# Optimization experiments

Measured on AMD Instinct MI355X. Metric: run time of the kernel, lower is better.

Reference implementation:

```python
import jax, jax.numpy as jnp
import numpy as np

B, V, S = 128, 64, 40
D, H, VOC = 256, 256, 20000


def setup_inputs() -> dict:
    key = jax.random.key(0)
    ks = jax.random.split(key, 26)
    g = lambda k, shp: (jax.random.normal(k, shp, dtype=jnp.float32) * 0.02)
    inp = {}
    inp['input_seqs'] = jax.random.randint(ks[0], (B, V, S), 0, VOC + 1)
    inp['mask'] = jnp.zeros((B, V), jnp.float32)
    inp['length'] = jax.random.randint(ks[1], (B,), 1, V + 1)
    inp['seq_time_step'] = jax.random.uniform(ks[2], (B, V), dtype=jnp.float32)
    inp['codemask'] = jnp.zeros((B, V, S), jnp.float32)
    inp['label'] = jax.random.randint(ks[3], (B,), 0, 2)
    # embedding table; padding_idx=-1 in torch == row VOC zeroed
    inp['emb'] = g(ks[4], (VOC + 1, D)).at[VOC].set(0.0)
    # LSTM (single layer, batch_first): torch gate order i,f,g,o
    inp['W_ih'] = g(ks[5], (4 * H, D))
    inp['W_hh'] = g(ks[6], (4 * H, H))
    inp['b_ih'] = g(ks[7], (4 * H,))
    inp['b_hh'] = g(ks[8], (4 * H,))
    # attention projections
    inp['Whk'] = g(ks[9], (D, H))
    inp['bhk'] = g(ks[10], (D,))
    inp['W1'] = g(ks[11], (64, 2 * H))
    inp['b1'] = g(ks[12], (64,))
    inp['W2'] = g(ks[13], (2, 64))
    inp['b2'] = g(ks[14], (2,))
    # classifyer MLP: d -> 4d -> 2d -> 2
    inp['C1W'] = g(ks[15], (4 * D, D))
    inp['C1b'] = g(ks[16], (4 * D,))
    inp['C2W'] = g(ks[17], (2 * D, 4 * D))
    inp['C2b'] = g(ks[18], (2 * D,))
    inp['CoW'] = g(ks[19], (2, 2 * D))
    inp['Cob'] = g(ks[20], (2,))
    return inp


def _lstm(x, W_ih, W_hh, b_ih, b_hh):
    # x: [B,T,D] -> hs: [B,T,H]; torch gate order i,f,g,o
    Bsz = x.shape[0]
    Hd = W_hh.shape[1]
    xg = jnp.einsum('btd,gd->btg', x, W_ih) + b_ih + b_hh  # [B,T,4H]

    def step(carry, xg_t):
        h, c = carry
        gates = xg_t + h @ W_hh.T
        i, f, gg, o = jnp.split(gates, 4, axis=-1)
        i = jax.nn.sigmoid(i); f = jax.nn.sigmoid(f)
        gg = jnp.tanh(gg); o = jax.nn.sigmoid(o)
        c = f * c + i * gg
        h = o * jnp.tanh(c)
        return (h, c), h

    z = jnp.zeros((Bsz, Hd), x.dtype)
    _, hs = jax.lax.scan(step, (z, z), jnp.swapaxes(xg, 0, 1))
    return jnp.swapaxes(hs, 0, 1)


def _classify(h, C1W, C1b, C2W, C2b, CoW, Cob):
    h = jax.nn.relu(h @ C1W.T + C1b)
    h = jax.nn.relu(h @ C2W.T + C2b)
    return h @ CoW.T + Cob


def reference(input_seqs, mask, length, seq_time_step, codemask, label,
              emb, W_ih, W_hh, b_ih, b_hh, Whk, bhk, W1, b1, W2, b2,
              C1W, C1b, C2W, C2b, CoW, Cob):
    # before(): embedding gather -> relu -> sum over codes (eval mode, no dropout)
    v = jax.nn.relu(emb[input_seqs]).sum(-2)  # [B,V,D]
    h = _lstm(v, W_ih, W_hh, b_ih, b_hh)       # [B,V,H]

    # vectorized form of the per-timestep attention loop:
    # bar_v[:,0]=v[:,0]; for i>=1: mix of e_k=v[:,0] and w_hk(h[:,i-1])
    e_k = v[:, :1, :]                                   # [B,1,D]
    wh = h @ Whk.T + bhk                                # [B,V,D]
    wh_prev = wh[:, :-1, :]                             # [B,V-1,D] (h at i-1)
    e_b = jnp.broadcast_to(e_k, wh_prev.shape)
    cat = jnp.concatenate([e_b, wh_prev], axis=-1)      # [B,V-1,2D]
    attn = jax.nn.softmax(jnp.tanh(cat @ W1.T + b1) @ W2.T + b2, axis=-1)
    bar_rest = e_b * attn[..., 0:1] + wh_prev * attn[..., 1:2]
    bar_v = jnp.concatenate([v[:, :1, :], bar_rest], axis=1)  # [B,V,D]

    # GAN stand-in (external injected module): identity
    Dec_V, Gen_V = bar_v, bar_v
    gen_h = _lstm(Gen_V, W_ih, W_hh, b_ih, b_hh)

    og = _classify(h, C1W, C1b, C2W, C2b, CoW, Cob)        # [B,V,2]
    fake = _classify(gen_h, C1W, C1b, C2W, C2b, CoW, Cob)  # [B,V,2]
    final_og = og[:, -1, :]
    final_fake = fake[:, -1, :]
    return (final_og, final_fake, Dec_V, Gen_V, seq_time_step, label)
```

## Files before the change

### kernel.cpp

```cpp
#include <hip/hip_runtime.h>

#define DEV __device__ __forceinline__

typedef float f32x4 __attribute__((ext_vector_type(4)));
typedef short s16x8 __attribute__((ext_vector_type(8)));
typedef short s16x4 __attribute__((ext_vector_type(4)));

DEV unsigned short f2bf(float f){
  unsigned int u = __float_as_uint(f);
  u += 0x7fffu + ((u>>16)&1u);
  return (unsigned short)(u>>16);
}
DEV float bf2f(unsigned short h){ return __uint_as_float(((unsigned int)h)<<16); }

#if __has_builtin(__builtin_amdgcn_rcpf)
DEV float frcp_(float x){ return __builtin_amdgcn_rcpf(x); }
#else
DEV float frcp_(float x){ return 1.f/x; }
#endif
#if __has_builtin(__builtin_amdgcn_exp2f)
DEV float fexp2_(float x){ return __builtin_amdgcn_exp2f(x); }
#else
DEV float fexp2_(float x){ return exp2f(x); }
#endif

DEV float tanh_(float x){
  x = fminf(x, 30.f);
  float e = fexp2_(2.8853900817779268f*x);
  return (e-1.f)*frcp_(e+1.f);
}

DEV unsigned char f2e4m3(float x){
  unsigned int u = __float_as_uint(x);
  unsigned int s = (u>>24)&0x80u;
  unsigned int mag = u & 0x7fffffffu;
  if (mag > 0x43E00000u) mag = 0x43E00000u;
  mag += 0x000FFFFFu + ((mag>>20)&1u);
  int e = (int)(mag>>23) - 120;
  unsigned int m = (mag>>20)&7u;
  unsigned int r = (e<=0) ? 0u : (((unsigned)e<<3)|m);
  return (unsigned char)(s|r);
}

DEV f32x4 mfma_bf16(s16x8 a, s16x8 b, f32x4 c){
  return __builtin_amdgcn_mfma_f32_16x16x32_bf16(a,b,c,0,0,0);
}
DEV f32x4 mfma_fp8(long a, long b, f32x4 c){
  return __builtin_amdgcn_mfma_f32_16x16x32_fp8_fp8(a,b,c,0,0,0);
}

DEV void lds_barrier(){
  asm volatile("s_waitcnt lgkmcnt(0)\n\ts_barrier" ::: "memory");
}

DEV unsigned aload_rlx(unsigned* p){
  return __hip_atomic_load(p, __ATOMIC_RELAXED, __HIP_MEMORY_SCOPE_AGENT);
}
DEV void astore_rel(unsigned* p, unsigned v){
  __hip_atomic_store(p, v, __ATOMIC_RELEASE, __HIP_MEMORY_SCOPE_AGENT);
}
DEV void aadd_rel(unsigned* p, unsigned v){
  __hip_atomic_fetch_add(p, v, __ATOMIC_RELEASE, __HIP_MEMORY_SCOPE_AGENT);
}
DEV void acq_fence(){ __builtin_amdgcn_fence(__ATOMIC_ACQUIRE, "agent"); }
DEV void spin_rlx(unsigned* p, unsigned tgt){
  while (aload_rlx(p) < tgt) __builtin_amdgcn_s_sleep(8);
  asm volatile("" ::: "memory");
}
template<int FENCE>
DEV void block_wait_ge(unsigned* p, unsigned tgt){
  if (threadIdx.x == 0){
    spin_rlx(p, tgt);
    if (FENCE) acq_fence();
  }
  __syncthreads();
}
DEV s16x4 aload64(const unsigned short* p){
  unsigned long long v = __hip_atomic_load((unsigned long long*)(void*)p,
      __ATOMIC_RELAXED, __HIP_MEMORY_SCOPE_AGENT);
  union { unsigned long long u; s16x4 s; } c; c.u = v; return c.s;
}

#define Bx 128
#define Vx 64
#define Sx 40
#define Dx 256
#define Hx 256
#define NVOC 20001

#define OFF_OG   0
#define OFF_FAKE 256
#define OFF_DECV 512
#define OFF_GENV 2097664
#define OFF_STS  4194816
#define OFF_LBL  4203008

#define PW_IH  0
#define PW_HH  262144
#define PW_HK  524288
#define PW_1   589824
#define PC_1   622592
#define PC_2   884736
#define PC_O   1409024
#define P_TOT  1410048

#define HPB 264
#define WHP 272

#define FCT(t) ((t)*32)
#define FBV(t) (2048 + (t)*32)
#define FXG(t) (4096 + (t)*32)
#define FUC    6144
#define FTOT   8192

__global__ void k_cvt_emb(const float* __restrict__ emb, unsigned short* __restrict__ emb16){
  size_t i = (size_t)blockIdx.x*256 + threadIdx.x;
  emb16[i] = f2bf(emb[i]);
}

__global__ void k_pre(const int* __restrict__ seqs, const unsigned short* __restrict__ emb16,
                      unsigned short* __restrict__ v16,
                      float* __restrict__ decv, float* __restrict__ genv,
                      unsigned short* __restrict__ barv16,
                      const float* __restrict__ W_ih, const float* __restrict__ Whh,
                      const float* __restrict__ Whk, const float* __restrict__ W1,
                      const float* __restrict__ C1W, const float* __restrict__ C2W,
                      const float* __restrict__ CoW,
                      unsigned short* __restrict__ pool, unsigned char* __restrict__ whh8,
                      const float* __restrict__ sts, const int* __restrict__ label,
                      float* __restrict__ out, unsigned* __restrict__ flags){
  int bx = blockIdx.x, tid = threadIdx.x;
  if (bx < 8192){
    int bt = bx, d = tid;
    const int* sp = seqs + (size_t)bt*Sx;
    float acc = 0.f;
    #pragma unroll 8
    for (int s=0;s<Sx;s++) acc += fmaxf(bf2f(emb16[(size_t)sp[s]*Dx + d]), 0.f);
    size_t o = (size_t)bt*Dx + d;
    v16[o] = f2bf(acc);
    if ((bt & 63) == 0){ decv[o] = acc; genv[o] = acc; barv16[o] = f2bf(acc); }
    return;
  }
  if (bx < 14724){
    int i = (bx-8192)*256 + tid;
    if (i < P_TOT){
      float v;
      if      (i < PW_HH) v = W_ih[i - PW_IH];
      else if (i < PW_HK) v = Whh [i - PW_HH];
      else if (i < PW_1 ) v = Whk [i - PW_HK];
      else if (i < PC_1 ) v = W1  [i - PW_1 ];
      else if (i < PC_2 ) v = C1W [i - PC_1 ];
      else if (i < PC_O ) v = C2W [i - PC_2 ];
      else                v = CoW [i - PC_O ];
      pool[i] = f2bf(v);
    } else if (i < P_TOT + 262144){
      whh8[i - P_TOT] = f2e4m3(16.f*Whh[i - P_TOT]);
    }
    return;
  }
  for (int i=tid;i<FTOT;i+=256) flags[i] = (i==FBV(0)) ? 1u : 0u;
  for (int i=tid;i<Bx*Vx;i+=256) out[OFF_STS + i] = sts[i];
  if (tid < Bx) out[OFF_LBL + tid] = (float)label[tid];
}

template<int MODE_A, int MODE_C, int RELU>
__global__ void k_gemm(const unsigned short* __restrict__ A, const unsigned short* __restrict__ Bw,
                       const float* __restrict__ bias1, const float* __restrict__ bias2,
                       unsigned short* __restrict__ C, int K, int Ntot, float scale){
  int tid = threadIdx.x, w = tid>>6, l = tid&63, lm = l&15, q = l>>4;
  int m0 = blockIdx.x*64;
  int n0 = blockIdx.y*256 + w*64;
  f32x4 acc[4][4];
  #pragma unroll
  for (int nt=0;nt<4;nt++){
    int n = n0 + nt*16 + lm;
    float bz = bias1 ? bias1[n] : 0.f;
    if (bias2) bz += bias2[n];
    #pragma unroll
    for (int mt=0;mt<4;mt++) acc[mt][nt] = (f32x4){bz,bz,bz,bz};
  }
  const s16x8* Arow[4];
  #pragma unroll
  for (int mt=0;mt<4;mt++){
    int m = m0 + mt*16 + lm;
    size_t off = (MODE_A==0) ? (size_t)m*K : ((size_t)(m&127)*Vx + (m>>7))*(size_t)K;
    Arow[mt] = (const s16x8*)(A + off);
  }
  int kkn = K/32;
  for (int kk=0; kk<kkn; kk++){
    s16x8 bfr[4];
    #pragma unroll
    for (int nt=0;nt<4;nt++){
      int n = n0 + nt*16 + lm;
      bfr[nt] = *(const s16x8*)(Bw + (size_t)n*K + kk*32 + q*8);
    }
    #pragma unroll
    for (int mt=0;mt<4;mt++){
      s16x8 afr = Arow[mt][kk*4 + q];
      #pragma unroll
      for (int nt=0;nt<4;nt++)
        acc[mt][nt] = mfma_bf16(afr, bfr[nt], acc[mt][nt]);
    }
  }
  #pragma unroll
  for (int mt=0;mt<4;mt++){
    int mbase = m0 + mt*16 + q*4;
    #pragma unroll
    for (int nt=0;nt<4;nt++){
      int n = n0 + nt*16 + lm;
      if (MODE_C==0){
        #pragma unroll
        for (int r=0;r<4;r++){
          float val = scale*acc[mt][nt][r];
          if (RELU) val = fmaxf(val, 0.f);
          C[(size_t)(mbase+r)*Ntot + n] = f2bf(val);
        }
      } else {
        int tt = mbase>>7, bb = mbase&127;
        int gg = bb>>4;
        s16x4 sv;
        #pragma unroll
        for (int r=0;r<4;r++) sv[r] = (short)f2bf(scale*acc[mt][nt][r]);
        *(s16x4*)(C + (((size_t)tt*8 + gg)*1024 + n)*16 + (bb&15)) = sv;
      }
    }
  }
}

template<int IS1>
DEV void scan_body(unsigned char* hl, const unsigned char* __restrict__ W8,
                   const unsigned short* __restrict__ xg, unsigned short* __restrict__ hist,
                   int g, unsigned* __restrict__ flags){
  int tid = threadIdx.x;
  int w = tid>>6, l = tid&63, lm = l&15, q = l>>4;
  int j = w*16 + lm;
  for (int i=tid;i<2*16*HPB;i+=1024) hl[i] = 0;
  long Bf[4][8];
  #pragma unroll
  for (int qq=0;qq<4;qq++){
    int n = qq*256 + j;
    #pragma unroll
    for (int kk=0;kk<8;kk++)
      Bf[qq][kk] = *(const long*)(W8 + (size_t)n*256 + kk*32 + q*8);
  }
  float cst[4] = {0.f,0.f,0.f,0.f};
  const unsigned short* xgb = xg + (size_t)g*16384 + q*4;
  s16x4 xc[4], xn[4];
  if (!IS1) block_wait_ge<0>(&flags[FXG(0)], 1);
  #pragma unroll
  for (int qq=0;qq<4;qq++){
    const unsigned short* p = xgb + (qq*256+j)*16;
    xc[qq] = IS1 ? *(const s16x4*)p : aload64(p);
  }
  __syncthreads();
  const float K1 = 1.4426950408889634f/256.f;
  const unsigned char* hrd = hl + lm*HPB + q*8;
  #pragma unroll 1
  for (int t=0;t<Vx;t++){
    if (t < Vx-1){
      if (!IS1) block_wait_ge<0>(&flags[FXG(t+1)], 1);
      #pragma unroll
      for (int qq=0;qq<4;qq++){
        const unsigned short* p = xgb + (size_t)(t+1)*131072 + (qq*256+j)*16;
        xn[qq] = IS1 ? *(const s16x4*)p : aload64(p);
      }
    }
    const unsigned char* hb = hrd + (t&1)*(16*HPB);
    f32x4 a0, a1, a2, a3;
    #pragma unroll
    for (int r=0;r<4;r++){
      a0[r] = bf2f((unsigned short)xc[0][r]);
      a1[r] = bf2f((unsigned short)xc[1][r]);
      a2[r] = bf2f((unsigned short)xc[2][r]);
      a3[r] = bf2f((unsigned short)xc[3][r]);
    }
    #pragma unroll
    for (int kk=0;kk<8;kk++){
      long af = *(const long*)(hb + kk*32);
      a0 = mfma_fp8(af, Bf[0][kk], a0);
      a1 = mfma_fp8(af, Bf[1][kk], a1);
      a2 = mfma_fp8(af, Bf[2][kk], a2);
      a3 = mfma_fp8(af, Bf[3][kk], a3);
    }
    unsigned char* hn = hl + ((t+1)&1)*(16*HPB) + j;
    float hv16[4];
    #pragma unroll
    for (int r=0;r<4;r++){
      float iv = frcp_(1.f + fexp2_(-K1*a0[r]));
      float fv = frcp_(1.f + fexp2_(-K1*a1[r]));
      float eg = fexp2_(2.f*K1*a2[r]);
      float gv = (eg-1.f)*frcp_(eg+1.f);
      float ov = frcp_(1.f + fexp2_(-K1*a3[r]));
      float cv = fv*cst[r] + iv*gv;
      cst[r] = cv;
      float ec = fexp2_(2.8853900817779268f*fminf(cv,30.f));
      float hv = ov*(ec-1.f)*frcp_(ec+1.f);
      hv16[r] = 16.f*hv;
      if (IS1)
        hist[((size_t)t*Bx + g*16 + q*4 + r)*Hx + j] = f2bf(hv);
      else if (t==Vx-1)
        hist[((size_t)(g*16 + q*4 + r))*Hx + j] = f2bf(hv);
    }
#if __has_builtin(__builtin_amdgcn_cvt_pk_fp8_f32)
    int p01 = __builtin_amdgcn_cvt_pk_fp8_f32(hv16[0], hv16[1], 0, false);
    int p23 = __builtin_amdgcn_cvt_pk_fp8_f32(hv16[2], hv16[3], 0, false);
    hn[(q*4+0)*HPB] = (unsigned char)p01;
    hn[(q*4+1)*HPB] = (unsigned char)(p01>>8);
    hn[(q*4+2)*HPB] = (unsigned char)p23;
    hn[(q*4+3)*HPB] = (unsigned char)(p23>>8);
#else
    #pragma unroll
    for (int r=0;r<4;r++) hn[(q*4+r)*HPB] = f2e4m3(hv16[r]);
#endif
    #pragma unroll
    for (int qq=0;qq<4;qq++) xc[qq] = xn[qq];
    if (IS1){
      __syncthreads();
      if (tid == 0) aadd_rel(&flags[FCT(t)], 1);
    } else {
      lds_barrier();
    }
  }
}

DEV void worker_body(unsigned short* whs, int t,
    const unsigned short* __restrict__ hist1, const unsigned short* __restrict__ v16,
    const float* __restrict__ u, const unsigned short* __restrict__ pool,
    const float* __restrict__ bhk, const float* __restrict__ W2, const float* __restrict__ b2,
    const float* __restrict__ b_ih, const float* __restrict__ b_hh,
    float* __restrict__ decv, float* __restrict__ genv,
    unsigned short* __restrict__ barv16, unsigned short* __restrict__ xg2,
    unsigned* flags){
  int tid = threadIdx.x, w = tid>>6, l = tid&63, lm = l&15, q = l>>4;
  if (t < 63){
    block_wait_ge<1>(&flags[FCT(t)], 8);
    int r0 = (w&7)*16, n0 = (w>>3)*128;
    const s16x8* Arow = (const s16x8*)(hist1 + ((size_t)t*Bx + r0 + lm)*Hx);
    f32x4 acc[8];
    #pragma unroll
    for (int nt=0;nt<8;nt++){
      float bz = bhk[n0 + nt*16 + lm];
      acc[nt] = (f32x4){bz,bz,bz,bz};
    }
    #pragma unroll
    for (int kk=0;kk<8;kk++){
      s16x8 afr = Arow[kk*4 + q];
      #pragma unroll
      for (int nt=0;nt<8;nt++){
        int n = n0 + nt*16 + lm;
        s16x8 bfr = *(const s16x8*)(pool + PW_HK + (size_t)n*256 + kk*32 + q*8);
        acc[nt] = mfma_bf16(afr, bfr, acc[nt]);
      }
    }
    #pragma unroll
    for (int nt=0;nt<8;nt++){
      int n = n0 + nt*16 + lm, mb = r0 + q*4;
      #pragma unroll
      for (int r=0;r<4;r++) whs[(size_t)(mb+r)*WHP + n] = f2bf(acc[nt][r]);
    }
    if (tid == 0){ spin_rlx(&flags[FUC], 8); acq_fence(); }
    __syncthreads();
    if (w < 8){
      int m0l = w*16;
      f32x4 a2[4];
      #pragma unroll
      for (int nt=0;nt<4;nt++){
        int n = nt*16 + lm;
        #pragma unroll
        for (int r=0;r<4;r++) a2[nt][r] = u[(size_t)(m0l + q*4 + r)*64 + n];
      }
      #pragma unroll
      for (int kk=0;kk<8;kk++){
        s16x8 afr = *(const s16x8*)(whs + (size_t)(m0l+lm)*WHP + kk*32 + q*8);
        #pragma unroll
        for (int nt=0;nt<4;nt++){
          int n = nt*16 + lm;
          s16x8 bfr = *(const s16x8*)(pool + PW_1 + (size_t)n*512 + 256 + kk*32 + q*8);
          a2[nt] = mfma_bf16(afr, bfr, a2[nt]);
        }
      }
      float p0a[4] = {0,0,0,0}, p1a[4] = {0,0,0,0};
      #pragma unroll
      for (int nt=0;nt<4;nt++){
        int n = nt*16 + lm;
        float w2a = W2[n], w2b = W2[64+n];
        #pragma unroll
        for (int r=0;r<4;r++){
          float z = tanh_(a2[nt][r]);
          p0a[r] += z*w2a; p1a[r] += z*w2b;
        }
      }
      #pragma unroll
      for (int s=1;s<16;s<<=1){
        #pragma unroll
        for (int r=0;r<4;r++){ p0a[r] += __shfl_xor(p0a[r], s, 16); p1a[r] += __shfl_xor(p1a[r], s, 16); }
      }
      float bb0 = b2[0], bb1 = b2[1];
      int d0 = lm*16;
      #pragma unroll
      for (int r=0;r<4;r++){
        int b = m0l + q*4 + r;
        float g0 = p0a[r]+bb0, g1 = p1a[r]+bb1;
        float al0 = frcp_(1.f + fexp2_(1.4426950408889634f*(g1-g0)));
        float al1 = 1.f - al0;
        const unsigned short* ek  = v16 + (size_t)b*Vx*Dx + d0;
        const unsigned short* whp = whs + (size_t)b*WHP + d0;
        size_t ob = ((size_t)b*Vx + (t+1))*Dx + d0;
        #pragma unroll
        for (int c=0;c<2;c++){
          s16x8 e8 = *(const s16x8*)(ek + c*8);
          s16x8 w8 = *(const s16x8*)(whp + c*8);
          s16x8 o16;
          #pragma unroll
          for (int jj=0;jj<8;jj++){
            float o = al0*bf2f((unsigned short)e8[jj]) + al1*bf2f((unsigned short)w8[jj]);
            decv[ob + c*8 + jj] = o;
            genv[ob + c*8 + jj] = o;
            o16[jj] = (short)f2bf(o);
          }
          *(s16x8*)(barv16 + ob + c*8) = o16;
        }
      }
    }
    __syncthreads();
    if (tid == 0) astore_rel(&flags[FBV(t+1)], 1);
  }
  block_wait_ge<1>(&flags[FBV(t)], 1);
  int mh = (w&1)*64, nb = (w>>1)*128;
  const s16x8* Arow2[4];
  #pragma unroll
  for (int mt=0;mt<4;mt++)
    Arow2[mt] = (const s16x8*)(barv16 + ((size_t)(mh + mt*16 + lm)*Vx + t)*Dx);
  #pragma unroll 1
  for (int sc=0; sc<4; sc++){
    int n0 = nb + sc*32;
    f32x4 acc[4][2];
    #pragma unroll
    for (int nt=0;nt<2;nt++){
      int n = n0 + nt*16 + lm;
      float bz = b_ih[n] + b_hh[n];
      #pragma unroll
      for (int mt=0;mt<4;mt++) acc[mt][nt] = (f32x4){bz,bz,bz,bz};
    }
    #pragma unroll
    for (int kk=0;kk<8;kk++){
      s16x8 bfr[2];
      #pragma unroll
      for (int nt=0;nt<2;nt++){
        int n = n0 + nt*16 + lm;
        bfr[nt] = *(const s16x8*)(pool + PW_IH + (size_t)n*256 + kk*32 + q*8);
      }
      #pragma unroll
      for (int mt=0;mt<4;mt++){
        s16x8 afr = Arow2[mt][kk*4 + q];
        acc[mt][0] = mfma_bf16(afr, bfr[0], acc[mt][0]);
        acc[mt][1] = mfma_bf16(afr, bfr[1], acc[mt][1]);
      }
    }
    #pragma unroll
    for (int mt=0;mt<4;mt++){
      int m = mh + mt*16 + q*4;
      int gg = m>>4;
      #pragma unroll
      for (int nt=0;nt<2;nt++){
        int n = n0 + nt*16 + lm;
        s16x4 sv;
        #pragma unroll
        for (int r=0;r<4;r++) sv[r] = (short)f2bf(256.f*acc[mt][nt][r]);
        *(s16x4*)(xg2 + (((size_t)t*8 + gg)*1024 + n)*16 + (m&15)) = sv;
      }
    }
  }
  __syncthreads();
  if (tid == 0) astore_rel(&flags[FXG(t)], 1);
}

__global__ __launch_bounds__(1024) void k_mega(
    const unsigned char* __restrict__ W8,
    const unsigned short* __restrict__ xg1, unsigned short* __restrict__ xg2,
    unsigned short* __restrict__ hist1, unsigned short* __restrict__ h2,
    const unsigned short* __restrict__ v16, float* __restrict__ u,
    const unsigned short* __restrict__ pool,
    const float* __restrict__ bhk, const float* __restrict__ W2, const float* __restrict__ b2,
    const float* __restrict__ b1, const float* __restrict__ b_ih, const float* __restrict__ b_hh,
    float* __restrict__ decv, float* __restrict__ genv, unsigned short* __restrict__ barv16,
    unsigned* __restrict__ flags){
  __shared__ __align__(16) unsigned char smem[69632];
  int blk = blockIdx.x;
  if (blk < 8){
    scan_body<1>(smem, W8, xg1, hist1, blk, flags);
  } else if (blk < 16){
    scan_body<0>(smem, W8, xg2, h2, blk-8, flags);
  } else if (blk < 80){
    worker_body((unsigned short*)smem, blk-16, hist1, v16, u, pool, bhk, W2, b2,
                b_ih, b_hh, decv, genv, barv16, xg2, flags);
  } else {
    int t2 = (blk-80)*1024 + threadIdx.x;
    int b = t2>>6, n = t2&63;
    const s16x8* vr = (const s16x8*)(v16 + (size_t)b*Vx*Dx);
    const s16x8* wr = (const s16x8*)(pool + PW_1 + (size_t)n*512);
    float a = b1[n];
    for (int kk=0;kk<32;kk++){
      s16x8 x = vr[kk], ww = wr[kk];
      #pragma unroll
      for (int jj=0;jj<8;jj++) a += bf2f((unsigned short)x[jj])*bf2f((unsigned short)ww[jj]);
    }
    u[t2] = a;
    __syncthreads();
    if (threadIdx.x == 0) aadd_rel(&flags[FUC], 1);
  }
}

__global__ void k_out(const unsigned short* __restrict__ y2, const unsigned short* __restrict__ CoW16,
                      const float* __restrict__ Cob, float* __restrict__ out){
  int tid = blockIdx.x*256 + threadIdx.x;
  int m = tid>>1, n = tid&1;
  const s16x8* yr = (const s16x8*)(y2 + (size_t)m*512);
  const s16x8* wr = (const s16x8*)(CoW16 + (size_t)n*512);
  float a = Cob[n];
  for (int kk=0;kk<64;kk++){
    s16x8 yv = yr[kk], ww = wr[kk];
    #pragma unroll
    for (int jj=0;jj<8;jj++) a += bf2f((unsigned short)yv[jj])*bf2f((unsigned short)ww[jj]);
  }
  int base = (m < 128) ? (OFF_OG + m*2) : (OFF_FAKE + (m-128)*2);
  out[base + n] = a;
}

extern "C" void kernel_launch(void* const* d_in, const int* in_sizes, int n_in,
                              void* d_out, int out_size, void* d_ws, size_t ws_size,
                              hipStream_t stream) {
  const int*   seqs  = (const int*)d_in[0];
  const float* sts   = (const float*)d_in[3];
  const int*   label = (const int*)d_in[5];
  const float* emb   = (const float*)d_in[6];
  const float* W_ih  = (const float*)d_in[7];
  const float* W_hh  = (const float*)d_in[8];
  const float* b_ih  = (const float*)d_in[9];
  const float* b_hh  = (const float*)d_in[10];
  const float* Whk   = (const float*)d_in[11];
  const float* bhk   = (const float*)d_in[12];
  const float* W1    = (const float*)d_in[13];
  const float* b1    = (const float*)d_in[14];
  const float* W2    = (const float*)d_in[15];
  const float* b2    = (const float*)d_in[16];
  const float* C1b   = (const float*)d_in[18];
  const float* C2b   = (const float*)d_in[20];
  const float* Cob   = (const float*)d_in[22];
  float* out = (float*)d_out;

  char* ws = (char*)d_ws;
  unsigned short* v16    = (unsigned short*)(ws + 0);
  unsigned short* xg1    = (unsigned short*)(ws + (4<<20));
  unsigned short* hist1  = (unsigned short*)(ws + (20<<20));
  unsigned short* barv16 = (unsigned short*)(ws + (25<<20));
  unsigned short* xg2    = (unsigned short*)(ws + (29<<20));
  unsigned short* emb16  = xg2;
  float*          u      = (float*)(ws + (45<<20));
  unsigned char*  whh8   = (unsigned char*)(ws + (45<<20) + (64<<10));
  unsigned*       flags  = (unsigned*)(ws + (45<<20) + (384<<10));
  unsigned short* pool   = (unsigned short*)(ws + (46<<20));
  unsigned short* y1     = xg1;
  unsigned short* y2     = xg1 + 262144;

  unsigned short* h2 = hist1 + (size_t)Vx*Bx*Hx;
  unsigned short* X  = hist1 + (size_t)(Vx-1)*Bx*Hx;

  float* decv = out + OFF_DECV;
  float* genv = out + OFF_GENV;

  k_cvt_emb<<<dim3(NVOC), dim3(256), 0, stream>>>(emb, emb16);
  k_pre<<<dim3(14725), dim3(256), 0, stream>>>(seqs, emb16, v16, decv, genv, barv16,
      W_ih, W_hh, Whk, W1, (const float*)d_in[17], (const float*)d_in[19],
      (const float*)d_in[21], pool, whh8, sts, label, out, flags);
  k_gemm<1,1,0><<<dim3(128,4), dim3(256), 0, stream>>>(v16, pool+PW_IH, b_ih, b_hh, xg1, 256, 1024, 256.f);
  k_mega<<<dim3(88), dim3(1024), 0, stream>>>(whh8, xg1, xg2, hist1, h2, v16, u, pool,
      bhk, W2, b2, b1, b_ih, b_hh, decv, genv, barv16, flags);
  k_gemm<0,0,1><<<dim3(4,4), dim3(256), 0, stream>>>(X, pool+PC_1, C1b, nullptr, y1, 256, 1024, 1.f);
  k_gemm<0,0,1><<<dim3(4,2), dim3(256), 0, stream>>>(y1, pool+PC_2, C2b, nullptr, y2, 1024, 512, 1.f);
  k_out<<<dim3(2), dim3(256), 0, stream>>>(y2, pool+PC_O, Cob, out);
}
```

Baseline: 539.7 us.

## Fuse attention-mix and xg2 GEMM per worker, use relaxed atomics for flags

Each worker block now computes the bar_v mix and immediately runs the W_ih GEMM for step t+1 from LDS, so the barv16 global buffer and the FBV handshake between workers go away. Cross-block synchronization switches from release/acquire fences to relaxed atomic loads and stores, with explicit vmcnt drains before each flag is raised. The scan stages h through LDS to emit coalesced 64-bit stores, the spin sleep interval is shortened, and decv/genv use nontemporal stores. The intent is to shorten the critical dependency chain and cut fence overhead. The risk is that memory-ordering correctness now rests on the vmcnt drains plus relaxed atomics rather than on proper acquire semantics.

```diff
diff --git a/kernel.cpp b/kernel.cpp
--- a/kernel.cpp
+++ b/kernel.cpp
@@ -56,23 +56,18 @@
 DEV unsigned aload_rlx(unsigned* p){
   return __hip_atomic_load(p, __ATOMIC_RELAXED, __HIP_MEMORY_SCOPE_AGENT);
 }
-DEV void astore_rel(unsigned* p, unsigned v){
-  __hip_atomic_store(p, v, __ATOMIC_RELEASE, __HIP_MEMORY_SCOPE_AGENT);
-}
-DEV void aadd_rel(unsigned* p, unsigned v){
-  __hip_atomic_fetch_add(p, v, __ATOMIC_RELEASE, __HIP_MEMORY_SCOPE_AGENT);
-}
-DEV void acq_fence(){ __builtin_amdgcn_fence(__ATOMIC_ACQUIRE, "agent"); }
+DEV void astore_rlx(unsigned* p, unsigned v){
+  __hip_atomic_store(p, v, __ATOMIC_RELAXED, __HIP_MEMORY_SCOPE_AGENT);
+}
+DEV void aadd_rlx(unsigned* p, unsigned v){
+  __hip_atomic_fetch_add(p, v, __ATOMIC_RELAXED, __HIP_MEMORY_SCOPE_AGENT);
+}
 DEV void spin_rlx(unsigned* p, unsigned tgt){
-  while (aload_rlx(p) < tgt) __builtin_amdgcn_s_sleep(8);
+  while (aload_rlx(p) < tgt) __builtin_amdgcn_s_sleep(2);
   asm volatile("" ::: "memory");
 }
-template<int FENCE>
-DEV void block_wait_ge(unsigned* p, unsigned tgt){
-  if (threadIdx.x == 0){
-    spin_rlx(p, tgt);
-    if (FENCE) acq_fence();
-  }
+DEV void block_wait(unsigned* p, unsigned tgt){
+  if (threadIdx.x == 0) spin_rlx(p, tgt);
   __syncthreads();
 }
 DEV s16x4 aload64(const unsigned short* p){
@@ -80,6 +75,26 @@
       __ATOMIC_RELAXED, __HIP_MEMORY_SCOPE_AGENT);
   union { unsigned long long u; s16x4 s; } c; c.u = v; return c.s;
 }
+DEV void astore64(unsigned short* p, s16x4 v){
+  union { s16x4 s; unsigned long long u; } c; c.s = v;
+  __hip_atomic_store((unsigned long long*)(void*)p, c.u,
+      __ATOMIC_RELAXED, __HIP_MEMORY_SCOPE_AGENT);
+}
+DEV s16x8 aload128(const unsigned short* p){
+  s16x4 a = aload64(p), b = aload64(p+4);
+  s16x8 r;
+  r[0]=a[0]; r[1]=a[1]; r[2]=a[2]; r[3]=a[3];
+  r[4]=b[0]; r[5]=b[1]; r[6]=b[2]; r[7]=b[3];
+  return r;
+}
+DEV float aloadf(const float* p){
+  return __hip_atomic_load((float*)(void*)p, __ATOMIC_RELAXED, __HIP_MEMORY_SCOPE_AGENT);
+}
+DEV void astoref(float* p, float v){
+  __hip_atomic_store(p, v, __ATOMIC_RELAXED, __HIP_MEMORY_SCOPE_AGENT);
+}
+DEV void vm_drain(){ asm volatile("s_waitcnt vmcnt(0)" ::: "memory"); }
+DEV void ntf(float* p, float v){ __builtin_nontemporal_store(v, p); }
 
 #define Bx 128
 #define Vx 64
@@ -105,13 +120,13 @@
 #define P_TOT  1410048
 
 #define HPB 264
+#define BFP 272
 #define WHP 272
 
 #define FCT(t) ((t)*32)
-#define FBV(t) (2048 + (t)*32)
-#define FXG(t) (4096 + (t)*32)
-#define FUC    6144
-#define FTOT   8192
+#define FXG(t) (2048 + (t)*32)
+#define FUC    4096
+#define FTOT   4224
 
 __global__ void k_cvt_emb(const float* __restrict__ emb, unsigned short* __restrict__ emb16){
   size_t i = (size_t)blockIdx.x*256 + threadIdx.x;
@@ -121,7 +136,6 @@
 __global__ void k_pre(const int* __restrict__ seqs, const unsigned short* __restrict__ emb16,
                       unsigned short* __restrict__ v16,
                       float* __restrict__ decv, float* __restrict__ genv,
-                      unsigned short* __restrict__ barv16,
                       const float* __restrict__ W_ih, const float* __restrict__ Whh,
                       const float* __restrict__ Whk, const float* __restrict__ W1,
                       const float* __restrict__ C1W, const float* __restrict__ C2W,
@@ -138,7 +152,7 @@
     for (int s=0;s<Sx;s++) acc += fmaxf(bf2f(emb16[(size_t)sp[s]*Dx + d]), 0.f);
     size_t o = (size_t)bt*Dx + d;
     v16[o] = f2bf(acc);
-    if ((bt & 63) == 0){ decv[o] = acc; genv[o] = acc; barv16[o] = f2bf(acc); }
+    if ((bt & 63) == 0){ decv[o] = acc; genv[o] = acc; }
     return;
   }
   if (bx < 14724){
@@ -158,7 +172,7 @@
     }
     return;
   }
-  for (int i=tid;i<FTOT;i+=256) flags[i] = (i==FBV(0)) ? 1u : 0u;
+  for (int i=tid;i<FTOT;i+=256) flags[i] = 0u;
   for (int i=tid;i<Bx*Vx;i+=256) out[OFF_STS + i] = sts[i];
   if (tid < Bx) out[OFF_LBL + tid] = (float)label[tid];
 }
@@ -227,14 +241,46 @@
   }
 }
 
+DEV void lstm_act(const f32x4* A, float* cst, float* hv){
+  const float K1 = 1.4426950408889634f/256.f;
+  #pragma unroll
+  for (int r=0;r<4;r++){
+    float iv = frcp_(1.f + fexp2_(-K1*A[0][r]));
+    float fv = frcp_(1.f + fexp2_(-K1*A[1][r]));
+    float eg = fexp2_(2.f*K1*A[2][r]);
+    float gv = (eg-1.f)*frcp_(eg+1.f);
+    float ov = frcp_(1.f + fexp2_(-K1*A[3][r]));
+    float cv = fv*cst[r] + iv*gv;
+    cst[r] = cv;
+    float ec = fexp2_(2.8853900817779268f*fminf(cv,30.f));
+    hv[r] = ov*(ec-1.f)*frcp_(ec+1.f);
+  }
+}
+
+DEV void store_h_fp8(unsigned char* hn, int q, const float* hv){
+#if __has_builtin(__builtin_amdgcn_cvt_pk_fp8_f32)
+  int p01 = __builtin_amdgcn_cvt_pk_fp8_f32(16.f*hv[0], 16.f*hv[1], 0, false);
+  int p23 = __builtin_amdgcn_cvt_pk_fp8_f32(16.f*hv[2], 16.f*hv[3], 0, false);
+  hn[(q*4+0)*HPB] = (unsigned char)p01;
+  hn[(q*4+1)*HPB] = (unsigned char)(p01>>8);
+  hn[(q*4+2)*HPB] = (unsigned char)p23;
+  hn[(q*4+3)*HPB] = (unsigned char)(p23>>8);
+#else
+  #pragma unroll
+  for (int r=0;r<4;r++) hn[(q*4+r)*HPB] = f2e4m3(16.f*hv[r]);
+#endif
+}
+
 template<int IS1>
-DEV void scan_body(unsigned char* hl, const unsigned char* __restrict__ W8,
+DEV void scan_body(unsigned char* smem, const unsigned char* __restrict__ W8,
                    const unsigned short* __restrict__ xg, unsigned short* __restrict__ hist,
                    int g, unsigned* __restrict__ flags){
+  unsigned char*  hl  = smem;
+  unsigned short* h1b = (unsigned short*)(smem + 8448);
   int tid = threadIdx.x;
   int w = tid>>6, l = tid&63, lm = l&15, q = l>>4;
   int j = w*16 + lm;
-  for (int i=tid;i<2*16*HPB;i+=1024) hl[i] = 0;
+  for (int i=tid;i<8448;i+=1024) hl[i] = 0;
   long Bf[4][8];
   #pragma unroll
   for (int qq=0;qq<4;qq++){
@@ -246,79 +292,112 @@
   float cst[4] = {0.f,0.f,0.f,0.f};
   const unsigned short* xgb = xg + (size_t)g*16384 + q*4;
   s16x4 xc[4], xn[4];
-  if (!IS1) block_wait_ge<0>(&flags[FXG(0)], 1);
+  if (!IS1) block_wait(&flags[FXG(0)], 1);
   #pragma unroll
   for (int qq=0;qq<4;qq++){
     const unsigned short* p = xgb + (qq*256+j)*16;
     xc[qq] = IS1 ? *(const s16x4*)p : aload64(p);
   }
   __syncthreads();
-  const float K1 = 1.4426950408889634f/256.f;
   const unsigned char* hrd = hl + lm*HPB + q*8;
   #pragma unroll 1
   for (int t=0;t<Vx;t++){
     if (t < Vx-1){
-      if (!IS1) block_wait_ge<0>(&flags[FXG(t+1)], 1);
+      if (!IS1) block_wait(&flags[FXG(t+1)], 1);
       #pragma unroll
       for (int qq=0;qq<4;qq++){
         const unsigned short* p = xgb + (size_t)(t+1)*131072 + (qq*256+j)*16;
         xn[qq] = IS1 ? *(const s16x4*)p : aload64(p);
       }
     }
-    const unsigned char* hb = hrd + (t&1)*(16*HPB);
-    f32x4 a0, a1, a2, a3;
-    #pragma unroll
-    for (int r=0;r<4;r++){
-      a0[r] = bf2f((unsigned short)xc[0][r]);
-      a1[r] = bf2f((unsigned short)xc[1][r]);
-      a2[r] = bf2f((unsigned short)xc[2][r]);
-      a3[r] = bf2f((unsigned short)xc[3][r]);
+    const unsigned char* hb = hrd + (t&1)*4224;
+    f32x4 A[4];
+    #pragma unroll
+    for (int qq=0;qq<4;qq++){
+      #pragma unroll
+      for (int r=0;r<4;r++) A[qq][r] = bf2f((unsigned short)xc[qq][r]);
     }
     #pragma unroll
     for (int kk=0;kk<8;kk++){
       long af = *(const long*)(hb + kk*32);
-      a0 = mfma_fp8(af, Bf[0][kk], a0);
-      a1 = mfma_fp8(af, Bf[1][kk], a1);
-      a2 = mfma_fp8(af, Bf[2][kk], a2);
-      a3 = mfma_fp8(af, Bf[3][kk], a3);
-    }
-    unsigned char* hn = hl + ((t+1)&1)*(16*HPB) + j;
-    float hv16[4];
-    #pragma unroll
-    for (int r=0;r<4;r++){
-      float iv = frcp_(1.f + fexp2_(-K1*a0[r]));
-      float fv = frcp_(1.f + fexp2_(-K1*a1[r]));
-      float eg = fexp2_(2.f*K1*a2[r]);
-      float gv = (eg-1.f)*frcp_(eg+1.f);
-      float ov = frcp_(1.f + fexp2_(-K1*a3[r]));
-      float cv = fv*cst[r] + iv*gv;
-      cst[r] = cv;
-      float ec = fexp2_(2.8853900817779268f*fminf(cv,30.f));
-      float hv = ov*(ec-1.f)*frcp_(ec+1.f);
-      hv16[r] = 16.f*hv;
-      if (IS1)
-        hist[((size_t)t*Bx + g*16 + q*4 + r)*Hx + j] = f2bf(hv);
-      else if (t==Vx-1)
-        hist[((size_t)(g*16 + q*4 + r))*Hx + j] = f2bf(hv);
-    }
-#if __has_builtin(__builtin_amdgcn_cvt_pk_fp8_f32)
-    int p01 = __builtin_amdgcn_cvt_pk_fp8_f32(hv16[0], hv16[1], 0, false);
-    int p23 = __builtin_amdgcn_cvt_pk_fp8_f32(hv16[2], hv16[3], 0, false);
-    hn[(q*4+0)*HPB] = (unsigned char)p01;
-    hn[(q*4+1)*HPB] = (unsigned char)(p01>>8);
-    hn[(q*4+2)*HPB] = (unsigned char)p23;
-    hn[(q*4+3)*HPB] = (unsigned char)(p23>>8);
-#else
-    #pragma unroll
-    for (int r=0;r<4;r++) hn[(q*4+r)*HPB] = f2e4m3(hv16[r]);
-#endif
+      A[0] = mfma_fp8(af, Bf[0][kk], A[0]);
+      A[1] = mfma_fp8(af, Bf[1][kk], A[1]);
+      A[2] = mfma_fp8(af, Bf[2][kk], A[2]);
+      A[3] = mfma_fp8(af, Bf[3][kk], A[3]);
+    }
+    float hv[4];
+    lstm_act(A, cst, hv);
+    store_h_fp8(hl + ((t+1)&1)*4224 + j, q, hv);
+    if (IS1){
+      #pragma unroll
+      for (int r=0;r<4;r++) h1b[(q*4+r)*BFP + j] = f2bf(hv[r]);
+      lds_barrier();
+      {
+        int row = tid>>6, c4 = (tid&63)*4;
+        s16x4 hx = *(const s16x4*)(h1b + row*BFP + c4);
+        astore64(hist + ((size_t)t*Bx + g*16 + row)*Hx + c4, hx);
+      }
+      vm_drain();
+      __syncthreads();
+      if (tid == 0) aadd_rlx(&flags[FCT(t)], 1);
+    } else {
+      if (t == Vx-1){
+        #pragma unroll
+        for (int r=0;r<4;r++)
+          hist[(size_t)(g*16 + q*4 + r)*Hx + j] = f2bf(hv[r]);
+      }
+      lds_barrier();
+    }
     #pragma unroll
     for (int qq=0;qq<4;qq++) xc[qq] = xn[qq];
-    if (IS1){
-      __syncthreads();
-      if (tid == 0) aadd_rel(&flags[FCT(t)], 1);
-    } else {
-      lds_barrier();
+  }
+}
+
+template<int ALDS>
+DEV void xg2_tile(const unsigned short* Ab, const unsigned short* __restrict__ pool,
+                  const float* __restrict__ b_ih, const float* __restrict__ b_hh,
+                  unsigned short* __restrict__ xg2, int tile, int w, int lm, int q){
+  int mh = (w&1)*64, nb = (w>>1)*128;
+  #pragma unroll 1
+  for (int sc=0; sc<4; sc++){
+    int n0 = nb + sc*32;
+    f32x4 acc[4][2];
+    #pragma unroll
+    for (int nt=0;nt<2;nt++){
+      int n = n0 + nt*16 + lm;
+      float bz = b_ih[n] + b_hh[n];
+      #pragma unroll
+      for (int mt=0;mt<4;mt++) acc[mt][nt] = (f32x4){bz,bz,bz,bz};
+    }
+    #pragma unroll
+    for (int kk=0;kk<8;kk++){
+      s16x8 bfr[2];
+      #pragma unroll
+      for (int nt=0;nt<2;nt++){
+        int n = n0 + nt*16 + lm;
+        bfr[nt] = *(const s16x8*)(pool + PW_IH + (size_t)n*256 + kk*32 + q*8);
+      }
+      #pragma unroll
+      for (int mt=0;mt<4;mt++){
+        int row = mh + mt*16 + lm;
+        s16x8 afr = ALDS ? *(const s16x8*)(Ab + (size_t)row*WHP + kk*32 + q*8)
+                         : *(const s16x8*)(Ab + (size_t)row*Vx*Dx + kk*32 + q*8);
+        acc[mt][0] = mfma_bf16(afr, bfr[0], acc[mt][0]);
+        acc[mt][1] = mfma_bf16(afr, bfr[1], acc[mt][1]);
+      }
+    }
+    #pragma unroll
+    for (int mt=0;mt<4;mt++){
+      int m = mh + mt*16 + q*4;
+      int gg = m>>4;
+      #pragma unroll
+      for (int nt=0;nt<2;nt++){
+        int n = n0 + nt*16 + lm;
+        s16x4 sv;
+        #pragma unroll
+        for (int r=0;r<4;r++) sv[r] = (short)f2bf(256.f*acc[mt][nt][r]);
+        astore64(xg2 + (((size_t)tile*8 + gg)*1024 + n)*16 + (m&15), sv);
+      }
     }
   }
 }
@@ -329,13 +408,19 @@
     const float* __restrict__ bhk, const float* __restrict__ W2, const float* __restrict__ b2,
     const float* __restrict__ b_ih, const float* __restrict__ b_hh,
     float* __restrict__ decv, float* __restrict__ genv,
-    unsigned short* __restrict__ barv16, unsigned short* __restrict__ xg2,
-    unsigned* flags){
+    unsigned short* __restrict__ xg2, unsigned* __restrict__ flags){
   int tid = threadIdx.x, w = tid>>6, l = tid&63, lm = l&15, q = l>>4;
-  if (t < 63){
-    block_wait_ge<1>(&flags[FCT(t)], 8);
+  if (t == 63){
+    xg2_tile<0>(v16, pool, b_ih, b_hh, xg2, 0, w, lm, q);
+    vm_drain();
+    __syncthreads();
+    if (tid == 0) astore_rlx(&flags[FXG(0)], 1);
+    return;
+  }
+  block_wait(&flags[FCT(t)], 8);
+  {
     int r0 = (w&7)*16, n0 = (w>>3)*128;
-    const s16x8* Arow = (const s16x8*)(hist1 + ((size_t)t*Bx + r0 + lm)*Hx);
+    const unsigned short* Ar = hist1 + ((size_t)t*Bx + r0 + lm)*Hx;
     f32x4 acc[8];
     #pragma unroll
     for (int nt=0;nt<8;nt++){
@@ -344,7 +429,7 @@
     }
     #pragma unroll
     for (int kk=0;kk<8;kk++){
-      s16x8 afr = Arow[kk*4 + q];
+      s16x8 afr = aload128(Ar + kk*32 + q*8);
       #pragma unroll
       for (int nt=0;nt<8;nt++){
         int n = n0 + nt*16 + lm;
@@ -358,121 +443,76 @@
       #pragma unroll
       for (int r=0;r<4;r++) whs[(size_t)(mb+r)*WHP + n] = f2bf(acc[nt][r]);
     }
-    if (tid == 0){ spin_rlx(&flags[FUC], 8); acq_fence(); }
-    __syncthreads();
-    if (w < 8){
-      int m0l = w*16;
-      f32x4 a2[4];
+  }
+  if (tid == 0) spin_rlx(&flags[FUC], 8);
+  __syncthreads();
+  if (w < 8){
+    int m0l = w*16;
+    f32x4 a2[4];
+    #pragma unroll
+    for (int nt=0;nt<4;nt++){
+      int n = nt*16 + lm;
+      #pragma unroll
+      for (int r=0;r<4;r++) a2[nt][r] = aloadf(u + (size_t)(m0l + q*4 + r)*64 + n);
+    }
+    #pragma unroll
+    for (int kk=0;kk<8;kk++){
+      s16x8 afr = *(const s16x8*)(whs + (size_t)(m0l+lm)*WHP + kk*32 + q*8);
       #pragma unroll
       for (int nt=0;nt<4;nt++){
         int n = nt*16 + lm;
+        s16x8 bfr = *(const s16x8*)(pool + PW_1 + (size_t)n*512 + 256 + kk*32 + q*8);
+        a2[nt] = mfma_bf16(afr, bfr, a2[nt]);
+      }
+    }
+    float p0a[4] = {0,0,0,0}, p1a[4] = {0,0,0,0};
+    #pragma unroll
+    for (int nt=0;nt<4;nt++){
+      int n = nt*16 + lm;
+      float w2a = W2[n], w2b = W2[64+n];
+      #pragma unroll
+      for (int r=0;r<4;r++){
+        float z = tanh_(a2[nt][r]);
+        p0a[r] += z*w2a; p1a[r] += z*w2b;
+      }
+    }
+    #pragma unroll
+    for (int s=1;s<16;s<<=1){
+      #pragma unroll
+      for (int r=0;r<4;r++){ p0a[r] += __shfl_xor(p0a[r], s, 16); p1a[r] += __shfl_xor(p1a[r], s, 16); }
+    }
+    float bb0 = b2[0], bb1 = b2[1];
+    int d0 = lm*16;
+    #pragma unroll
+    for (int r=0;r<4;r++){
+      int b = m0l + q*4 + r;
+      float g0 = p0a[r]+bb0, g1 = p1a[r]+bb1;
+      float al0 = frcp_(1.f + fexp2_(1.4426950408889634f*(g1-g0)));
+      float al1 = 1.f - al0;
+      const unsigned short* ek = v16 + (size_t)b*Vx*Dx + d0;
+      unsigned short* whp = whs + (size_t)b*WHP + d0;
+      size_t ob = ((size_t)b*Vx + (t+1))*Dx + d0;
+      #pragma unroll
+      for (int c=0;c<2;c++){
+        s16x8 e8 = *(const s16x8*)(ek + c*8);
+        s16x8 w8 = *(const s16x8*)(whp + c*8);
+        s16x8 o16;
         #pragma unroll
-        for (int r=0;r<4;r++) a2[nt][r] = u[(size_t)(m0l + q*4 + r)*64 + n];
-      }
-      #pragma unroll
-      for (int kk=0;kk<8;kk++){
-        s16x8 afr = *(const s16x8*)(whs + (size_t)(m0l+lm)*WHP + kk*32 + q*8);
-        #pragma unroll
-        for (int nt=0;nt<4;nt++){
-          int n = nt*16 + lm;
-          s16x8 bfr = *(const s16x8*)(pool + PW_1 + (size_t)n*512 + 256 + kk*32 + q*8);
-          a2[nt] = mfma_bf16(afr, bfr, a2[nt]);
+        for (int jj=0;jj<8;jj++){
+          float o = al0*bf2f((unsigned short)e8[jj]) + al1*bf2f((unsigned short)w8[jj]);
+          ntf(decv + ob + c*8 + jj, o);
+          ntf(genv + ob + c*8 + jj, o);
+          o16[jj] = (short)f2bf(o);
         }
-      }
-      float p0a[4] = {0,0,0,0}, p1a[4] = {0,0,0,0};
-      #pragma unroll
-      for (int nt=0;nt<4;nt++){
-        int n = nt*16 + lm;
-        float w2a = W2[n], w2b = W2[64+n];
-        #pragma unroll
-        for (int r=0;r<4;r++){
-          float z = tanh_(a2[nt][r]);
-          p0a[r] += z*w2a; p1a[r] += z*w2b;
-        }
-      }
-      #pragma unroll
-      for (int s=1;s<16;s<<=1){
-        #pragma unroll
-        for (int r=0;r<4;r++){ p0a[r] += __shfl_xor(p0a[r], s, 16); p1a[r] += __shfl_xor(p1a[r], s, 16); }
-      }
-      float bb0 = b2[0], bb1 = b2[1];
-      int d0 = lm*16;
-      #pragma unroll
-      for (int r=0;r<4;r++){
-        int b = m0l + q*4 + r;
-        float g0 = p0a[r]+bb0, g1 = p1a[r]+bb1;
-        float al0 = frcp_(1.f + fexp2_(1.4426950408889634f*(g1-g0)));
-        float al1 = 1.f - al0;
-        const unsigned short* ek  = v16 + (size_t)b*Vx*Dx + d0;
-        const unsigned short* whp = whs + (size_t)b*WHP + d0;
-        size_t ob = ((size_t)b*Vx + (t+1))*Dx + d0;
-        #pragma unroll
-        for (int c=0;c<2;c++){
-          s16x8 e8 = *(const s16x8*)(ek + c*8);
-          s16x8 w8 = *(const s16x8*)(whp + c*8);
-          s16x8 o16;
-          #pragma unroll
-          for (int jj=0;jj<8;jj++){
-            float o = al0*bf2f((unsigned short)e8[jj]) + al1*bf2f((unsigned short)w8[jj]);
-            decv[ob + c*8 + jj] = o;
-            genv[ob + c*8 + jj] = o;
-            o16[jj] = (short)f2bf(o);
-          }
-          *(s16x8*)(barv16 + ob + c*8) = o16;
-        }
-      }
-    }
-    __syncthreads();
-    if (tid == 0) astore_rel(&flags[FBV(t+1)], 1);
-  }
-  block_wait_ge<1>(&flags[FBV(t)], 1);
-  int mh = (w&1)*64, nb = (w>>1)*128;
-  const s16x8* Arow2[4];
-  #pragma unroll
-  for (int mt=0;mt<4;mt++)
-    Arow2[mt] = (const s16x8*)(barv16 + ((size_t)(mh + mt*16 + lm)*Vx + t)*Dx);
-  #pragma unroll 1
-  for (int sc=0; sc<4; sc++){
-    int n0 = nb + sc*32;
-    f32x4 acc[4][2];
-    #pragma unroll
-    for (int nt=0;nt<2;nt++){
-      int n = n0 + nt*16 + lm;
-      float bz = b_ih[n] + b_hh[n];
-      #pragma unroll
-      for (int mt=0;mt<4;mt++) acc[mt][nt] = (f32x4){bz,bz,bz,bz};
-    }
-    #pragma unroll
-    for (int kk=0;kk<8;kk++){
-      s16x8 bfr[2];
-      #pragma unroll
-      for (int nt=0;nt<2;nt++){
-        int n = n0 + nt*16 + lm;
-        bfr[nt] = *(const s16x8*)(pool + PW_IH + (size_t)n*256 + kk*32 + q*8);
-      }
-      #pragma unroll
-      for (int mt=0;mt<4;mt++){
-        s16x8 afr = Arow2[mt][kk*4 + q];
-        acc[mt][0] = mfma_bf16(afr, bfr[0], acc[mt][0]);
-        acc[mt][1] = mfma_bf16(afr, bfr[1], acc[mt][1]);
-      }
-    }
-    #pragma unroll
-    for (int mt=0;mt<4;mt++){
-      int m = mh + mt*16 + q*4;
-      int gg = m>>4;
-      #pragma unroll
-      for (int nt=0;nt<2;nt++){
-        int n = n0 + nt*16 + lm;
-        s16x4 sv;
-        #pragma unroll
-        for (int r=0;r<4;r++) sv[r] = (short)f2bf(256.f*acc[mt][nt][r]);
-        *(s16x4*)(xg2 + (((size_t)t*8 + gg)*1024 + n)*16 + (m&15)) = sv;
+        *(s16x8*)(whp + c*8) = o16;
       }
     }
   }
   __syncthreads();
-  if (tid == 0) astore_rel(&flags[FXG(t)], 1);
+  xg2_tile<1>(whs, pool, b_ih, b_hh, xg2, t+1, w, lm, q);
+  vm_drain();
+  __syncthreads();
+  if (tid == 0) astore_rlx(&flags[FXG(t+1)], 1);
 }
 
 __global__ __launch_bounds__(1024) void k_mega(
@@ -483,7 +523,7 @@
     const unsigned short* __restrict__ pool,
     const float* __restrict__ bhk, const float* __restrict__ W2, const float* __restrict__ b2,
     const float* __restrict__ b1, const float* __restrict__ b_ih, const float* __restrict__ b_hh,
-    float* __restrict__ decv, float* __restrict__ genv, unsigned short* __restrict__ barv16,
+    float* __restrict__ decv, float* __restrict__ genv,
     unsigned* __restrict__ flags){
   __shared__ __align__(16) unsigned char smem[69632];
   int blk = blockIdx.x;
@@ -493,7 +533,7 @@
     scan_body<0>(smem, W8, xg2, h2, blk-8, flags);
   } else if (blk < 80){
     worker_body((unsigned short*)smem, blk-16, hist1, v16, u, pool, bhk, W2, b2,
-                b_ih, b_hh, decv, genv, barv16, xg2, flags);
+                b_ih, b_hh, decv, genv, xg2, flags);
   } else {
     int t2 = (blk-80)*1024 + threadIdx.x;
     int b = t2>>6, n = t2&63;
@@ -505,9 +545,10 @@
       #pragma unroll
       for (int jj=0;jj<8;jj++) a += bf2f((unsigned short)x[jj])*bf2f((unsigned short)ww[jj]);
     }
-    u[t2] = a;
+    astoref(u + t2, a);
+    vm_drain();
     __syncthreads();
-    if (threadIdx.x == 0) aadd_rel(&flags[FUC], 1);
+    if (threadIdx.x == 0) aadd_rlx(&flags[FUC], 1);
   }
 }
 
@@ -553,13 +594,12 @@
   unsigned short* v16    = (unsigned short*)(ws + 0);
   unsigned short* xg1    = (unsigned short*)(ws + (4<<20));
   unsigned short* hist1  = (unsigned short*)(ws + (20<<20));
-  unsigned short* barv16 = (unsigned short*)(ws + (25<<20));
-  unsigned short* xg2    = (unsigned short*)(ws + (29<<20));
+  unsigned short* xg2    = (unsigned short*)(ws + (25<<20));
   unsigned short* emb16  = xg2;
-  float*          u      = (float*)(ws + (45<<20));
-  unsigned char*  whh8   = (unsigned char*)(ws + (45<<20) + (64<<10));
-  unsigned*       flags  = (unsigned*)(ws + (45<<20) + (384<<10));
-  unsigned short* pool   = (unsigned short*)(ws + (46<<20));
+  float*          u      = (float*)(ws + (41<<20));
+  unsigned char*  whh8   = (unsigned char*)(ws + (41<<20) + (64<<10));
+  unsigned*       flags  = (unsigned*)(ws + (41<<20) + (384<<10));
+  unsigned short* pool   = (unsigned short*)(ws + (42<<20));
   unsigned short* y1     = xg1;
   unsigned short* y2     = xg1 + 262144;
 
@@ -570,12 +610,12 @@
   float* genv = out + OFF_GENV;
 
   k_cvt_emb<<<dim3(NVOC), dim3(256), 0, stream>>>(emb, emb16);
-  k_pre<<<dim3(14725), dim3(256), 0, stream>>>(seqs, emb16, v16, decv, genv, barv16,
+  k_pre<<<dim3(14725), dim3(256), 0, stream>>>(seqs, emb16, v16, decv, genv,
       W_ih, W_hh, Whk, W1, (const float*)d_in[17], (const float*)d_in[19],
       (const float*)d_in[21], pool, whh8, sts, label, out, flags);
   k_gemm<1,1,0><<<dim3(128,4), dim3(256), 0, stream>>>(v16, pool+PW_IH, b_ih, b_hh, xg1, 256, 1024, 256.f);
   k_mega<<<dim3(88), dim3(1024), 0, stream>>>(whh8, xg1, xg2, hist1, h2, v16, u, pool,
-      bhk, W2, b2, b1, b_ih, b_hh, decv, genv, barv16, flags);
+      bhk, W2, b2, b1, b_ih, b_hh, decv, genv, flags);
   k_gemm<0,0,1><<<dim3(4,4), dim3(256), 0, stream>>>(X, pool+PC_1, C1b, nullptr, y1, 256, 1024, 1.f);
   k_gemm<0,0,1><<<dim3(4,2), dim3(256), 0, stream>>>(y1, pool+PC_2, C2b, nullptr, y2, 1024, 512, 1.f);
   k_out<<<dim3(2), dim3(256), 0, stream>>>(y2, pool+PC_O, Cob, out);
```

Result: faster. 484.8 us (-10.2%).
